# Kernel tuning notes

Hardware: AMD Instinct MI355X
Metric: run time of the kernel (lower is better)

## Reference

```python
import jax, jax.numpy as jnp
import numpy as np

BETA = 0.25
EPS = 1e-12

def normalise(x):
    # L2 normalise over last axis
    return x / jnp.sqrt(jnp.sum(x * x, axis=-1, keepdims=True) + EPS)

def setup_inputs() -> dict:
    key = jax.random.key(0)
    k = jax.random.split(key, 6)
    N, d, c, P = 8192, 768, 256, 16384
    return {
        "z": jax.random.normal(k[0], (N, d), dtype=jnp.float32),
        "W_in": jax.random.normal(k[1], (d, c), dtype=jnp.float32) * 0.02,
        "b_in": jnp.zeros((c,), dtype=jnp.float32),
        "W_out": jax.random.normal(k[2], (c, d), dtype=jnp.float32) * 0.02,
        "b_out": jnp.zeros((d,), dtype=jnp.float32),
        "codebook": jax.random.normal(k[3], (P, c), dtype=jnp.float32),
    }

def reference(z, W_in, b_in, W_out, b_out, codebook):
    sg = jax.lax.stop_gradient
    # input projection + L2 normalise
    zq = normalise(z @ W_in + b_in)                 # [N, c]
    cb = normalise(codebook)                        # [P, c]
    # squared euclidean distances: ||z||^2 - 2 z.c + ||c||^2
    dist = (jnp.sum(zq * zq, axis=-1, keepdims=True)
            - 2.0 * jnp.einsum('nc,pc->np', zq, cb)
            + jnp.sum(cb * cb, axis=-1)[None, :])   # [N, P]
    idxes = jnp.argmin(dist, axis=-1)               # [N]
    codes = normalise(codebook[idxes])              # gather + normalise, [N, c]
    loss = BETA * (zq - sg(codes)) ** 2 + (sg(zq) - codes) ** 2
    # straight-through estimator
    codes = zq + sg(codes - zq)
    out = codes @ W_out + b_out                     # [N, d]
    return out, loss, idxes
```

## Files before the change

### kernel.cpp

```cpp
#include <hip/hip_runtime.h>
#include <hip/hip_fp16.h>
#include <math.h>

#define NN 8192
#define DD 768
#define CC 256
#define PP 16384
#define NG 256
#define MARGIN 5.0e-3f
#define BETA_C 1.25f
#define EPS_C 1e-12f

typedef __attribute__((ext_vector_type(8))) _Float16 f16x8;
typedef __attribute__((ext_vector_type(8))) short bf16x8;
typedef __attribute__((ext_vector_type(4))) float f32x4;
typedef __attribute__((ext_vector_type(16))) float f32x16;

static __device__ __forceinline__ ushort f2h(float x) {
    _Float16 h = (_Float16)x;
    return __builtin_bit_cast(unsigned short, h);
}
static __device__ __forceinline__ ushort f2bf(float x) {
    unsigned u = __float_as_uint(x);
    return (ushort)((u + 0x7fffu + ((u >> 16) & 1u)) >> 16);
}

static __device__ __forceinline__ void gload_lds16(const void* g, void* l) {
    __builtin_amdgcn_global_load_lds(
        (const __attribute__((address_space(1))) unsigned int*)g,
        (__attribute__((address_space(3))) unsigned int*)l, 16, 0, 0);
}

__global__ __launch_bounds__(256) void k_gemm_in(const float* __restrict__ z,
    const float* __restrict__ W, const float* __restrict__ b,
    float* __restrict__ zq)
{
    __shared__ float zt[64][36];
    __shared__ float wt[32][68];
    const int t = threadIdx.x;
    const int ti = t >> 4, tj = t & 15;
    const int n0 = blockIdx.x * 64;
    const int c0 = blockIdx.y * 64;

    f32x4 acc[4];
#pragma unroll
    for (int r = 0; r < 4; ++r) acc[r] = (f32x4){0.f, 0.f, 0.f, 0.f};

    for (int k0 = 0; k0 < DD; k0 += 32) {
        __syncthreads();
#pragma unroll
        for (int l = 0; l < 2; ++l) {
            int idx = l * 256 + t;
            int row = idx >> 3, c4 = idx & 7;
            *reinterpret_cast<float4*>(&zt[row][c4 * 4]) =
                *reinterpret_cast<const float4*>(&z[(size_t)(n0 + row) * DD + k0 + c4 * 4]);
            int krow = idx >> 4, w4 = idx & 15;
            *reinterpret_cast<float4*>(&wt[krow][w4 * 4]) =
                *reinterpret_cast<const float4*>(&W[(size_t)(k0 + krow) * CC + c0 + w4 * 4]);
        }
        __syncthreads();
#pragma unroll
        for (int kk = 0; kk < 32; kk += 4) {
            float4 a4[4], b4[4];
#pragma unroll
            for (int r = 0; r < 4; ++r)
                a4[r] = *reinterpret_cast<const float4*>(&zt[ti * 4 + r][kk]);
#pragma unroll
            for (int q = 0; q < 4; ++q)
                b4[q] = *reinterpret_cast<const float4*>(&wt[kk + q][tj * 4]);
#pragma unroll
            for (int q = 0; q < 4; ++q)
#pragma unroll
                for (int r = 0; r < 4; ++r) {
                    float av = ((const float*)&a4[r])[q];
                    acc[r].x += av * b4[q].x;
                    acc[r].y += av * b4[q].y;
                    acc[r].z += av * b4[q].z;
                    acc[r].w += av * b4[q].w;
                }
        }
    }
#pragma unroll
    for (int r = 0; r < 4; ++r) {
        int col = c0 + tj * 4;
        float4 o;
        o.x = acc[r].x + b[col];
        o.y = acc[r].y + b[col + 1];
        o.z = acc[r].z + b[col + 2];
        o.w = acc[r].w + b[col + 3];
        *reinterpret_cast<float4*>(&zq[(size_t)(n0 + ti * 4 + r) * CC + col]) = o;
    }
}

__global__ __launch_bounds__(256) void k_norm2(const float* __restrict__ src,
    float* __restrict__ dstf32, ushort* __restrict__ dsth, int rows)
{
    const int wave = threadIdx.x >> 6;
    const int lane = threadIdx.x & 63;
    const int row = blockIdx.x * 4 + wave;
    if (row >= rows) return;
    float4 v = *reinterpret_cast<const float4*>(&src[(size_t)row * CC + lane * 4]);
    float s = v.x * v.x + v.y * v.y + v.z * v.z + v.w * v.w;
#pragma unroll
    for (int off = 32; off; off >>= 1) s += __shfl_xor(s, off, 64);
    float r = 1.0f / sqrtf(s + EPS_C);
    v.x *= r; v.y *= r; v.z *= r; v.w *= r;
    *reinterpret_cast<float4*>(&dstf32[(size_t)row * CC + lane * 4]) = v;
    ushort4 hv;
    hv.x = f2h(v.x); hv.y = f2h(v.y); hv.z = f2h(v.z); hv.w = f2h(v.w);
    *reinterpret_cast<ushort4*>(&dsth[(size_t)row * CC + lane * 4]) = hv;
}

__global__ __launch_bounds__(256) void k_prep(const float* __restrict__ codebook,
    ushort* __restrict__ cbh, float* __restrict__ cz2, float* __restrict__ rinv,
    const float* __restrict__ W, ushort* __restrict__ wthi)
{
    __shared__ float tile[64][68];
    const int t = threadIdx.x;
    if (blockIdx.x < 4096) {
        const int wave = t >> 6;
        const int lane = t & 63;
        const int row = blockIdx.x * 4 + wave;
        float4 v = *reinterpret_cast<const float4*>(&codebook[(size_t)row * CC + lane * 4]);
        float s = v.x * v.x + v.y * v.y + v.z * v.z + v.w * v.w;
#pragma unroll
        for (int off = 32; off; off >>= 1) s += __shfl_xor(s, off, 64);
        float r = 1.0f / sqrtf(s + EPS_C);
        v.x *= r; v.y *= r; v.z *= r; v.w *= r;
        ushort4 hv;
        hv.x = f2h(v.x); hv.y = f2h(v.y); hv.z = f2h(v.z); hv.w = f2h(v.w);
        *reinterpret_cast<ushort4*>(&cbh[(size_t)row * CC + lane * 4]) = hv;
        float s2 = v.x * v.x + v.y * v.y + v.z * v.z + v.w * v.w;
#pragma unroll
        for (int off = 32; off; off >>= 1) s2 += __shfl_xor(s2, off, 64);
        if (lane == 0) {
            cz2[row] = s2;
            rinv[row] = r;
        }
    } else {
        const int id = blockIdx.x - 4096;
        const int d0 = (id % 12) * 64;
        const int k0 = (id / 12) * 64;
#pragma unroll
        for (int i = 0; i < 16; ++i) {
            int row = i * 4 + (t >> 6);
            int col = t & 63;
            tile[row][col] = W[(size_t)(k0 + row) * DD + d0 + col];
        }
        __syncthreads();
#pragma unroll
        for (int i = 0; i < 16; ++i) {
            int drow = i * 4 + (t >> 6);
            int kc = t & 63;
            wthi[(size_t)(d0 + drow) * CC + k0 + kc] = f2bf(tile[kc][drow]);
        }
    }
}

__global__ __launch_bounds__(256, 4) void k_dist(
    const ushort* __restrict__ cbh, const ushort* __restrict__ zqh,
    const float* __restrict__ cz2,
    float* __restrict__ gmin, unsigned long long* __restrict__ maskA)
{
    __shared__ ushort lds[2][8192];
    const int t = threadIdx.x;
    const int lane = t & 63;
    const int w = t >> 6;
    const int wr = w >> 1;
    const int wc = w & 1;

    const int id = blockIdx.x;
    const int l = (id & 7) * 1024 + (id >> 3);
    const int p0 = (l >> 6) * 128;
    const int n0 = (l & 63) * 128;

    const int kh = lane >> 5;
    const int r31 = lane & 31;

    f32x16 acc[2][2];
#pragma unroll
    for (int mi = 0; mi < 2; ++mi) {
        const int pbm = p0 + wr * 64 + mi * 32;
#pragma unroll
        for (int q = 0; q < 4; ++q) {
            float4 cz = *reinterpret_cast<const float4*>(&cz2[pbm + q * 8 + kh * 4]);
#pragma unroll
            for (int j = 0; j < 4; ++j) {
                float v = -0.5f * ((const float*)&cz.x)[j];
                acc[mi][0][q * 4 + j] = v;
                acc[mi][1][q * 4 + j] = v;
            }
        }
    }

    const int u_l = lane >> 3;
    const int e = (lane & 7) ^ u_l;
    const int hh = e >> 2, jj = e & 3;
    const ushort* srcA[2];
    const ushort* srcB[2];
#pragma unroll
    for (int i = 0; i < 2; ++i)
        srcA[i] = cbh + (size_t)(p0 + 2 * (w * 16 + i * 8 + u_l) + hh) * CC + jj * 8;
#pragma unroll
    for (int i = 0; i < 2; ++i)
        srcB[i] = zqh + (size_t)(n0 + 2 * (w * 16 + i * 8 + u_l) + hh) * CC + jj * 8;

#define STAGE(BUF, KT)                                                        \
    {                                                                         \
        _Pragma("unroll")                                                     \
        for (int i = 0; i < 2; ++i)                                           \
            gload_lds16(srcA[i] + (KT) * 32, &lds[BUF][(w * 16 + i * 8) * 64]); \
        _Pragma("unroll")                                                     \
        for (int i = 0; i < 2; ++i)                                           \
            gload_lds16(srcB[i] + (KT) * 32, &lds[BUF][4096 + (w * 16 + i * 8) * 64]); \
    }

    const int ua = wr * 32 + (r31 >> 1);
    const int ub = wc * 32 + (r31 >> 1);
    const int hb = (r31 & 1) * 4 + kh;

#define COMPUTE(BUF)                                                          \
    {                                                                         \
        _Pragma("unroll")                                                     \
        for (int ks = 0; ks < 2; ++ks) {                                      \
            f16x8 af[2], bfv[2];                                              \
            _Pragma("unroll")                                                 \
            for (int mi = 0; mi < 2; ++mi) {                                  \
                int u = ua + mi * 16;                                         \
                af[mi] = *reinterpret_cast<const f16x8*>(                     \
                    &lds[BUF][u * 64 + (((hb + ks * 2) ^ (u & 7)) * 8)]);     \
            }                                                                 \
            _Pragma("unroll")                                                 \
            for (int ni = 0; ni < 2; ++ni) {                                  \
                int u = ub + ni * 16;                                         \
                bfv[ni] = *reinterpret_cast<const f16x8*>(                    \
                    &lds[BUF][4096 + u * 64 + (((hb + ks * 2) ^ (u & 7)) * 8)]); \
            }                                                                 \
            __builtin_amdgcn_s_setprio(1);                                    \
            acc[0][0] = __builtin_amdgcn_mfma_f32_32x32x16_f16(af[0], bfv[0], acc[0][0], 0, 0, 0); \
            acc[0][1] = __builtin_amdgcn_mfma_f32_32x32x16_f16(af[0], bfv[1], acc[0][1], 0, 0, 0); \
            acc[1][0] = __builtin_amdgcn_mfma_f32_32x32x16_f16(af[1], bfv[0], acc[1][0], 0, 0, 0); \
            acc[1][1] = __builtin_amdgcn_mfma_f32_32x32x16_f16(af[1], bfv[1], acc[1][1], 0, 0, 0); \
            __builtin_amdgcn_s_setprio(0);                                    \
        }                                                                     \
    }

#define BODY(KT, VM, DOSTAGE)                                                 \
    {                                                                         \
        if (DOSTAGE) STAGE(((KT) + 1) & 1, (KT) + 1);                         \
        __builtin_amdgcn_sched_barrier(0);                                    \
        asm volatile("s_waitcnt vmcnt(" #VM ")" ::: "memory");                \
        __builtin_amdgcn_s_barrier();                                         \
        __builtin_amdgcn_sched_barrier(0);                                    \
        COMPUTE((KT) & 1);                                                    \
        if ((KT) < 7) __builtin_amdgcn_s_barrier();                           \
    }

    STAGE(0, 0);
    BODY(0, 4, 1)
    BODY(1, 4, 1)
    BODY(2, 4, 1)
    BODY(3, 4, 1)
    BODY(4, 4, 1)
    BODY(5, 4, 1)
    BODY(6, 4, 1)
    BODY(7, 0, 0)

#undef BODY
#undef COMPUTE
#undef STAGE

#pragma unroll
    for (int ni = 0; ni < 2; ++ni) {
        float M = -1e30f;
#pragma unroll
        for (int mi = 0; mi < 2; ++mi)
#pragma unroll
            for (int r = 0; r < 16; ++r) M = fmaxf(M, acc[mi][ni][r]);
        M = fmaxf(M, __shfl_xor(M, 32, 64));
        const float thr = M - 0.5f * MARGIN;
        unsigned long long msk = 0ull;
#pragma unroll
        for (int mi = 0; mi < 2; ++mi)
#pragma unroll
            for (int q = 0; q < 4; ++q) {
                unsigned nib = 0u;
#pragma unroll
                for (int j = 0; j < 4; ++j)
                    nib |= (acc[mi][ni][q * 4 + j] >= thr) ? (1u << j) : 0u;
                msk |= (unsigned long long)nib << (mi * 32 + q * 8 + kh * 4);
            }
        msk |= __shfl_xor(msk, 32, 64);
        if (kh == 0) {
            int n = n0 + wc * 64 + ni * 32 + r31;
            int grp = (p0 >> 6) + wr;
            gmin[(size_t)n * NG + grp] = -2.0f * M;
            maskA[(size_t)n * NG + grp] = msk;
        }
    }
}

__global__ __launch_bounds__(256) void k_pick(
    const float* __restrict__ gmin, const unsigned long long* __restrict__ maskA,
    const float* __restrict__ zqn, const float* __restrict__ cb_raw,
    const float* __restrict__ rinv, const float* __restrict__ cz2,
    float* __restrict__ idxf, ushort* __restrict__ chi, float* __restrict__ loss)
{
    __shared__ int lst[4][256];
    __shared__ int cnt[4];
    const int t = threadIdx.x;
    const int w = t >> 6;
    const int lane = t & 63;
    const int row = blockIdx.x * 4 + w;

    float4 zr = *reinterpret_cast<const float4*>(&zqn[(size_t)row * CC + lane * 4]);
    float4 gv = *reinterpret_cast<const float4*>(&gmin[(size_t)row * NG + lane * 4]);

    float pm = fminf(fminf(gv.x, gv.y), fminf(gv.z, gv.w));
#pragma unroll
    for (int off = 1; off < 64; off <<= 1) pm = fminf(pm, __shfl_xor(pm, off, 64));
    const float thresh = pm + MARGIN;

    if (lane == 0) cnt[w] = 0;
    __syncthreads();
    {
        const float g4[4] = {gv.x, gv.y, gv.z, gv.w};
#pragma unroll
        for (int j = 0; j < 4; ++j)
            if (g4[j] <= thresh) {
                int pos = atomicAdd(&cnt[w], 1);
                lst[w][pos] = lane * 4 + j;
            }
    }
    __syncthreads();

    const int nc = cnt[w];
    unsigned long long best = ~0ull;
    for (int ci = 0; ci < nc; ++ci) {
        int g = lst[w][ci];
        unsigned long long msk = maskA[(size_t)row * NG + g];
        while (msk) {
            int bit = __ffsll((long long)msk) - 1;
            msk &= msk - 1;
            int p = g * 64 + bit;
            float rv = rinv[p];
            float4 c4 = *reinterpret_cast<const float4*>(&cb_raw[(size_t)p * CC + lane * 4]);
            float part = (c4.x * rv) * zr.x + (c4.y * rv) * zr.y
                       + (c4.z * rv) * zr.z + (c4.w * rv) * zr.w;
#pragma unroll
            for (int off = 1; off < 64; off <<= 1) part += __shfl_xor(part, off, 64);
            float d4 = fmaf(-2.0f, part, 4.0f + cz2[p]);
            unsigned long long pk = ((unsigned long long)__float_as_uint(d4) << 32) | (unsigned)p;
            best = best < pk ? best : pk;
        }
    }
    const int p = (int)(best & 0xffffffffu);
    if (lane == 0) idxf[row] = (float)p;

    const float rv = rinv[p];
    float4 cv = *reinterpret_cast<const float4*>(&cb_raw[(size_t)p * CC + lane * 4]);
    cv.x *= rv; cv.y *= rv; cv.z *= rv; cv.w *= rv;
    ushort4 hv;
    hv.x = f2bf(cv.x); hv.y = f2bf(cv.y); hv.z = f2bf(cv.z); hv.w = f2bf(cv.w);
    *reinterpret_cast<ushort4*>(&chi[(size_t)row * CC + lane * 4]) = hv;
    float4 lsv;
    float dx = zr.x - cv.x, dy = zr.y - cv.y, dz = zr.z - cv.z, dw = zr.w - cv.w;
    lsv.x = BETA_C * dx * dx; lsv.y = BETA_C * dy * dy;
    lsv.z = BETA_C * dz * dz; lsv.w = BETA_C * dw * dw;
    *reinterpret_cast<float4*>(&loss[(size_t)row * CC + lane * 4]) = lsv;
}

__global__ __launch_bounds__(256) void k_gemm_out_mfma(
    const ushort* __restrict__ chi, const ushort* __restrict__ wthi,
    const float* __restrict__ bout, float* __restrict__ out)
{
    __shared__ ushort sAh[128 * 64];
    __shared__ ushort sBh[128 * 64];
    const int t = threadIdx.x;
    const int lane = t & 63;
    const int w = t >> 6;
    const int wr = w >> 1;
    const int wc = w & 1;
    const int nb = blockIdx.x * 128;
    const int db = blockIdx.y * 128;
    const int kh = lane >> 5;
    const int r31 = lane & 31;

    f32x16 acc[2][2];
#pragma unroll
    for (int mi = 0; mi < 2; ++mi)
#pragma unroll
        for (int ni = 0; ni < 2; ++ni)
#pragma unroll
            for (int r = 0; r < 16; ++r) acc[mi][ni][r] = 0.f;

    const int srow = lane >> 3;
    const int schunk = (lane & 7) ^ srow;
    const size_t rowA = (size_t)(nb + w * 32 + srow) * CC;
    const size_t rowB = (size_t)(db + w * 32 + srow) * CC;
    const char* sAhsrc = (const char*)chi + rowA * 2 + schunk * 16;
    const char* sBhsrc = (const char*)wthi + rowB * 2 + schunk * 16;
    char* dA = (char*)sAh + (w * 32) * 128;
    char* dB = (char*)sBh + (w * 32) * 128;

    const int sx = (r31 & 7) << 4;

    for (int k0 = 0; k0 < CC; k0 += 64) {
        __syncthreads();
#pragma unroll
        for (int i = 0; i < 4; ++i) {
            gload_lds16(sAhsrc + (size_t)i * 8 * (CC * 2) + k0 * 2, dA + i * 1024);
            gload_lds16(sBhsrc + (size_t)i * 8 * (CC * 2) + k0 * 2, dB + i * 1024);
        }
        __syncthreads();
#pragma unroll
        for (int ks = 0; ks < 4; ++ks) {
            const int ko = ((ks * 32 + kh * 16) ^ sx);
            bf16x8 ah[2], bh[2];
#pragma unroll
            for (int mi = 0; mi < 2; ++mi)
                ah[mi] = *reinterpret_cast<const bf16x8*>(
                    (const char*)sAh + (wr * 64 + mi * 32 + r31) * 128 + ko);
#pragma unroll
            for (int ni = 0; ni < 2; ++ni)
                bh[ni] = *reinterpret_cast<const bf16x8*>(
                    (const char*)sBh + (wc * 64 + ni * 32 + r31) * 128 + ko);
#pragma unroll
            for (int mi = 0; mi < 2; ++mi)
#pragma unroll
                for (int ni = 0; ni < 2; ++ni)
                    acc[mi][ni] = __builtin_amdgcn_mfma_f32_32x32x16_bf16(
                        ah[mi], bh[ni], acc[mi][ni], 0, 0, 0);
        }
    }

#pragma unroll
    for (int ni = 0; ni < 2; ++ni) {
        const int d = db + wc * 64 + ni * 32 + r31;
        const float bv = bout[d];
#pragma unroll
        for (int mi = 0; mi < 2; ++mi) {
            const int nbase = nb + wr * 64 + mi * 32 + 4 * kh;
#pragma unroll
            for (int q = 0; q < 4; ++q)
#pragma unroll
                for (int j = 0; j < 4; ++j) {
                    int n = nbase + j + 8 * q;
                    out[(size_t)n * DD + d] = acc[mi][ni][q * 4 + j] + bv;
                }
        }
    }
}

extern "C" void kernel_launch(void* const* d_in, const int* in_sizes, int n_in,
                              void* d_out, int out_size, void* d_ws, size_t ws_size,
                              hipStream_t stream)
{
    const float* z        = (const float*)d_in[0];
    const float* W_in     = (const float*)d_in[1];
    const float* b_in     = (const float*)d_in[2];
    const float* W_out    = (const float*)d_in[3];
    const float* b_out    = (const float*)d_in[4];
    const float* codebook = (const float*)d_in[5];

    char* ws = (char*)d_ws;
    ushort* zqh   = (ushort*)(ws);
    ushort* cbh   = (ushort*)(ws + 4194304);
    ushort* chi   = (ushort*)(ws + 12582912);
    ushort* wthi  = (ushort*)(ws + 16777216);
    float*  cz2   = (float*)(ws + 17170432);
    float*  rinv  = (float*)(ws + 17235968);

    float* out  = (float*)d_out;
    float* loss = out + (size_t)NN * DD;
    float* idxf = loss + (size_t)NN * CC;

    float* gmin = (float*)d_out;
    unsigned long long* maskA = (unsigned long long*)((char*)d_out + 8388608);
    float* zq = loss;

    k_gemm_in<<<dim3(NN / 64, CC / 64), 256, 0, stream>>>(z, W_in, b_in, zq);
    k_norm2<<<NN / 4, 256, 0, stream>>>(zq, zq, zqh, NN);
    k_prep<<<PP / 4 + 48, 256, 0, stream>>>(codebook, cbh, cz2, rinv, W_out, wthi);
    k_dist<<<(PP / 128) * (NN / 128), 256, 0, stream>>>(cbh, zqh, cz2, gmin, maskA);
    k_pick<<<NN / 4, 256, 0, stream>>>(gmin, maskA, zq, codebook, rinv, cz2,
                                       idxf, chi, loss);
    k_gemm_out_mfma<<<dim3(NN / 128, DD / 128), 256, 0, stream>>>(chi, wthi, b_out, out);
}
```

Measured before the change: 192.3 us.

## Fuse input GEMM with L2 normalise and enlarge distance kernel P-tile

The input projection kernel now computes a full 256-wide row per block of 16 rows, so it can apply the bias, L2-normalise and write both fp32 and fp16 outputs directly. This removes the separate normalisation kernel and its extra round trip through global memory. The distance kernel's codebook tile is doubled from 128 to 256 rows, so each wave issues 8 MFMAs per k-step and zq tiles are reused more. In exchange it uses more registers and LDS, drops the occupancy hint and the block swizzle for L2 locality, and the input GEMM now does less work per thread and reloads the whole W slice in every block.

```diff
diff --git a/kernel.cpp b/kernel.cpp
--- a/kernel.cpp
+++ b/kernel.cpp
@@ -13,7 +13,6 @@
 
 typedef __attribute__((ext_vector_type(8))) _Float16 f16x8;
 typedef __attribute__((ext_vector_type(8))) short bf16x8;
-typedef __attribute__((ext_vector_type(4))) float f32x4;
 typedef __attribute__((ext_vector_type(16))) float f32x16;
 
 static __device__ __forceinline__ ushort f2h(float x) {
@@ -31,84 +30,84 @@
         (__attribute__((address_space(3))) unsigned int*)l, 16, 0, 0);
 }
 
-__global__ __launch_bounds__(256) void k_gemm_in(const float* __restrict__ z,
+__global__ __launch_bounds__(256) void k_gemm_in_norm(const float* __restrict__ z,
     const float* __restrict__ W, const float* __restrict__ b,
-    float* __restrict__ zq)
-{
-    __shared__ float zt[64][36];
-    __shared__ float wt[32][68];
+    float* __restrict__ zq, ushort* __restrict__ zqh)
+{
+    __shared__ float zt[16][36];
+    __shared__ float wt[32][260];
     const int t = threadIdx.x;
     const int ti = t >> 4, tj = t & 15;
-    const int n0 = blockIdx.x * 64;
-    const int c0 = blockIdx.y * 64;
-
-    f32x4 acc[4];
-#pragma unroll
-    for (int r = 0; r < 4; ++r) acc[r] = (f32x4){0.f, 0.f, 0.f, 0.f};
+    const int n0 = blockIdx.x * 16;
+
+    float acc[16];
+#pragma unroll
+    for (int c = 0; c < 16; ++c) acc[c] = 0.f;
 
     for (int k0 = 0; k0 < DD; k0 += 32) {
         __syncthreads();
-#pragma unroll
-        for (int l = 0; l < 2; ++l) {
-            int idx = l * 256 + t;
-            int row = idx >> 3, c4 = idx & 7;
+        if (t < 128) {
+            int row = t >> 3, c4 = t & 7;
             *reinterpret_cast<float4*>(&zt[row][c4 * 4]) =
                 *reinterpret_cast<const float4*>(&z[(size_t)(n0 + row) * DD + k0 + c4 * 4]);
-            int krow = idx >> 4, w4 = idx & 15;
+        }
+#pragma unroll
+        for (int l = 0; l < 8; ++l) {
+            int idx = l * 256 + t;
+            int krow = idx >> 6, w4 = idx & 63;
             *reinterpret_cast<float4*>(&wt[krow][w4 * 4]) =
-                *reinterpret_cast<const float4*>(&W[(size_t)(k0 + krow) * CC + c0 + w4 * 4]);
+                *reinterpret_cast<const float4*>(&W[(size_t)(k0 + krow) * CC + w4 * 4]);
         }
         __syncthreads();
 #pragma unroll
         for (int kk = 0; kk < 32; kk += 4) {
-            float4 a4[4], b4[4];
-#pragma unroll
-            for (int r = 0; r < 4; ++r)
-                a4[r] = *reinterpret_cast<const float4*>(&zt[ti * 4 + r][kk]);
-#pragma unroll
-            for (int q = 0; q < 4; ++q)
-                b4[q] = *reinterpret_cast<const float4*>(&wt[kk + q][tj * 4]);
-#pragma unroll
-            for (int q = 0; q < 4; ++q)
-#pragma unroll
-                for (int r = 0; r < 4; ++r) {
-                    float av = ((const float*)&a4[r])[q];
-                    acc[r].x += av * b4[q].x;
-                    acc[r].y += av * b4[q].y;
-                    acc[r].z += av * b4[q].z;
-                    acc[r].w += av * b4[q].w;
+            float4 a4 = *reinterpret_cast<const float4*>(&zt[ti][kk]);
+#pragma unroll
+            for (int q = 0; q < 4; ++q) {
+                float av = ((const float*)&a4)[q];
+#pragma unroll
+                for (int c = 0; c < 4; ++c) {
+                    float4 wv = *reinterpret_cast<const float4*>(&wt[kk + q][c * 64 + tj * 4]);
+                    acc[c * 4 + 0] += av * wv.x;
+                    acc[c * 4 + 1] += av * wv.y;
+                    acc[c * 4 + 2] += av * wv.z;
+                    acc[c * 4 + 3] += av * wv.w;
                 }
-        }
-    }
-#pragma unroll
-    for (int r = 0; r < 4; ++r) {
-        int col = c0 + tj * 4;
-        float4 o;
-        o.x = acc[r].x + b[col];
-        o.y = acc[r].y + b[col + 1];
-        o.z = acc[r].z + b[col + 2];
-        o.w = acc[r].w + b[col + 3];
-        *reinterpret_cast<float4*>(&zq[(size_t)(n0 + ti * 4 + r) * CC + col]) = o;
-    }
-}
-
-__global__ __launch_bounds__(256) void k_norm2(const float* __restrict__ src,
-    float* __restrict__ dstf32, ushort* __restrict__ dsth, int rows)
-{
-    const int wave = threadIdx.x >> 6;
-    const int lane = threadIdx.x & 63;
-    const int row = blockIdx.x * 4 + wave;
-    if (row >= rows) return;
-    float4 v = *reinterpret_cast<const float4*>(&src[(size_t)row * CC + lane * 4]);
-    float s = v.x * v.x + v.y * v.y + v.z * v.z + v.w * v.w;
-#pragma unroll
-    for (int off = 32; off; off >>= 1) s += __shfl_xor(s, off, 64);
-    float r = 1.0f / sqrtf(s + EPS_C);
-    v.x *= r; v.y *= r; v.z *= r; v.w *= r;
-    *reinterpret_cast<float4*>(&dstf32[(size_t)row * CC + lane * 4]) = v;
-    ushort4 hv;
-    hv.x = f2h(v.x); hv.y = f2h(v.y); hv.z = f2h(v.z); hv.w = f2h(v.w);
-    *reinterpret_cast<ushort4*>(&dsth[(size_t)row * CC + lane * 4]) = hv;
+            }
+        }
+    }
+
+    float p[4];
+#pragma unroll
+    for (int c = 0; c < 4; ++c) {
+        const int col = c * 64 + tj * 4;
+        acc[c * 4 + 0] += b[col + 0];
+        acc[c * 4 + 1] += b[col + 1];
+        acc[c * 4 + 2] += b[col + 2];
+        acc[c * 4 + 3] += b[col + 3];
+        p[c] = acc[c * 4 + 0] * acc[c * 4 + 0] + acc[c * 4 + 1] * acc[c * 4 + 1]
+             + acc[c * 4 + 2] * acc[c * 4 + 2] + acc[c * 4 + 3] * acc[c * 4 + 3];
+    }
+    float s0 = p[0] + p[2];
+    float s1 = p[1] + p[3];
+    float s = s0 + s1;
+#pragma unroll
+    for (int off = 8; off; off >>= 1) s += __shfl_xor(s, off, 64);
+    const float r = 1.0f / sqrtf(s + EPS_C);
+
+#pragma unroll
+    for (int c = 0; c < 4; ++c) {
+        const int col = c * 64 + tj * 4;
+        float4 v;
+        v.x = acc[c * 4 + 0] * r;
+        v.y = acc[c * 4 + 1] * r;
+        v.z = acc[c * 4 + 2] * r;
+        v.w = acc[c * 4 + 3] * r;
+        *reinterpret_cast<float4*>(&zq[(size_t)(n0 + ti) * CC + col]) = v;
+        ushort4 hv;
+        hv.x = f2h(v.x); hv.y = f2h(v.y); hv.z = f2h(v.z); hv.w = f2h(v.w);
+        *reinterpret_cast<ushort4*>(&zqh[(size_t)(n0 + ti) * CC + col]) = hv;
+    }
 }
 
 __global__ __launch_bounds__(256) void k_prep(const float* __restrict__ codebook,
@@ -157,30 +156,26 @@
     }
 }
 
-__global__ __launch_bounds__(256, 4) void k_dist(
+__global__ __launch_bounds__(256) void k_dist(
     const ushort* __restrict__ cbh, const ushort* __restrict__ zqh,
     const float* __restrict__ cz2,
     float* __restrict__ gmin, unsigned long long* __restrict__ maskA)
 {
-    __shared__ ushort lds[2][8192];
+    __shared__ ushort lds[2][12288];
     const int t = threadIdx.x;
     const int lane = t & 63;
     const int w = t >> 6;
     const int wr = w >> 1;
     const int wc = w & 1;
-
-    const int id = blockIdx.x;
-    const int l = (id & 7) * 1024 + (id >> 3);
-    const int p0 = (l >> 6) * 128;
-    const int n0 = (l & 63) * 128;
-
+    const int p0 = blockIdx.x * 256;
+    const int n0 = blockIdx.y * 128;
     const int kh = lane >> 5;
     const int r31 = lane & 31;
 
-    f32x16 acc[2][2];
-#pragma unroll
-    for (int mi = 0; mi < 2; ++mi) {
-        const int pbm = p0 + wr * 64 + mi * 32;
+    f32x16 acc[4][2];
+#pragma unroll
+    for (int mi = 0; mi < 4; ++mi) {
+        const int pbm = p0 + wr * 128 + mi * 32;
 #pragma unroll
         for (int q = 0; q < 4; ++q) {
             float4 cz = *reinterpret_cast<const float4*>(&cz2[pbm + q * 8 + kh * 4]);
@@ -196,11 +191,11 @@
     const int u_l = lane >> 3;
     const int e = (lane & 7) ^ u_l;
     const int hh = e >> 2, jj = e & 3;
-    const ushort* srcA[2];
+    const ushort* srcA[4];
     const ushort* srcB[2];
 #pragma unroll
-    for (int i = 0; i < 2; ++i)
-        srcA[i] = cbh + (size_t)(p0 + 2 * (w * 16 + i * 8 + u_l) + hh) * CC + jj * 8;
+    for (int i = 0; i < 4; ++i)
+        srcA[i] = cbh + (size_t)(p0 + 2 * (w * 32 + i * 8 + u_l) + hh) * CC + jj * 8;
 #pragma unroll
     for (int i = 0; i < 2; ++i)
         srcB[i] = zqh + (size_t)(n0 + 2 * (w * 16 + i * 8 + u_l) + hh) * CC + jj * 8;
@@ -208,14 +203,14 @@
 #define STAGE(BUF, KT)                                                        \
     {                                                                         \
         _Pragma("unroll")                                                     \
-        for (int i = 0; i < 2; ++i)                                           \
-            gload_lds16(srcA[i] + (KT) * 32, &lds[BUF][(w * 16 + i * 8) * 64]); \
+        for (int i = 0; i < 4; ++i)                                           \
+            gload_lds16(srcA[i] + (KT) * 32, &lds[BUF][(w * 32 + i * 8) * 64]); \
         _Pragma("unroll")                                                     \
         for (int i = 0; i < 2; ++i)                                           \
-            gload_lds16(srcB[i] + (KT) * 32, &lds[BUF][4096 + (w * 16 + i * 8) * 64]); \
-    }
-
-    const int ua = wr * 32 + (r31 >> 1);
+            gload_lds16(srcB[i] + (KT) * 32, &lds[BUF][8192 + (w * 16 + i * 8) * 64]); \
+    }
+
+    const int ua = wr * 64 + (r31 >> 1);
     const int ub = wc * 32 + (r31 >> 1);
     const int hb = (r31 & 1) * 4 + kh;
 
@@ -223,9 +218,9 @@
     {                                                                         \
         _Pragma("unroll")                                                     \
         for (int ks = 0; ks < 2; ++ks) {                                      \
-            f16x8 af[2], bfv[2];                                              \
+            f16x8 af[4], bfv[2];                                              \
             _Pragma("unroll")                                                 \
-            for (int mi = 0; mi < 2; ++mi) {                                  \
+            for (int mi = 0; mi < 4; ++mi) {                                  \
                 int u = ua + mi * 16;                                         \
                 af[mi] = *reinterpret_cast<const f16x8*>(                     \
                     &lds[BUF][u * 64 + (((hb + ks * 2) ^ (u & 7)) * 8)]);     \
@@ -234,13 +229,17 @@
             for (int ni = 0; ni < 2; ++ni) {                                  \
                 int u = ub + ni * 16;                                         \
                 bfv[ni] = *reinterpret_cast<const f16x8*>(                    \
-                    &lds[BUF][4096 + u * 64 + (((hb + ks * 2) ^ (u & 7)) * 8)]); \
+                    &lds[BUF][8192 + u * 64 + (((hb + ks * 2) ^ (u & 7)) * 8)]); \
             }                                                                 \
             __builtin_amdgcn_s_setprio(1);                                    \
             acc[0][0] = __builtin_amdgcn_mfma_f32_32x32x16_f16(af[0], bfv[0], acc[0][0], 0, 0, 0); \
             acc[0][1] = __builtin_amdgcn_mfma_f32_32x32x16_f16(af[0], bfv[1], acc[0][1], 0, 0, 0); \
             acc[1][0] = __builtin_amdgcn_mfma_f32_32x32x16_f16(af[1], bfv[0], acc[1][0], 0, 0, 0); \
             acc[1][1] = __builtin_amdgcn_mfma_f32_32x32x16_f16(af[1], bfv[1], acc[1][1], 0, 0, 0); \
+            acc[2][0] = __builtin_amdgcn_mfma_f32_32x32x16_f16(af[2], bfv[0], acc[2][0], 0, 0, 0); \
+            acc[2][1] = __builtin_amdgcn_mfma_f32_32x32x16_f16(af[2], bfv[1], acc[2][1], 0, 0, 0); \
+            acc[3][0] = __builtin_amdgcn_mfma_f32_32x32x16_f16(af[3], bfv[0], acc[3][0], 0, 0, 0); \
+            acc[3][1] = __builtin_amdgcn_mfma_f32_32x32x16_f16(af[3], bfv[1], acc[3][1], 0, 0, 0); \
             __builtin_amdgcn_s_setprio(0);                                    \
         }                                                                     \
     }
@@ -257,13 +256,13 @@
     }
 
     STAGE(0, 0);
-    BODY(0, 4, 1)
-    BODY(1, 4, 1)
-    BODY(2, 4, 1)
-    BODY(3, 4, 1)
-    BODY(4, 4, 1)
-    BODY(5, 4, 1)
-    BODY(6, 4, 1)
+    BODY(0, 6, 1)
+    BODY(1, 6, 1)
+    BODY(2, 6, 1)
+    BODY(3, 6, 1)
+    BODY(4, 6, 1)
+    BODY(5, 6, 1)
+    BODY(6, 6, 1)
     BODY(7, 0, 0)
 
 #undef BODY
@@ -272,30 +271,33 @@
 
 #pragma unroll
     for (int ni = 0; ni < 2; ++ni) {
-        float M = -1e30f;
-#pragma unroll
-        for (int mi = 0; mi < 2; ++mi)
-#pragma unroll
-            for (int r = 0; r < 16; ++r) M = fmaxf(M, acc[mi][ni][r]);
-        M = fmaxf(M, __shfl_xor(M, 32, 64));
-        const float thr = M - 0.5f * MARGIN;
-        unsigned long long msk = 0ull;
-#pragma unroll
-        for (int mi = 0; mi < 2; ++mi)
-#pragma unroll
-            for (int q = 0; q < 4; ++q) {
-                unsigned nib = 0u;
-#pragma unroll
-                for (int j = 0; j < 4; ++j)
-                    nib |= (acc[mi][ni][q * 4 + j] >= thr) ? (1u << j) : 0u;
-                msk |= (unsigned long long)nib << (mi * 32 + q * 8 + kh * 4);
+#pragma unroll
+        for (int g = 0; g < 2; ++g) {
+            float M = -1e30f;
+#pragma unroll
+            for (int m2 = 0; m2 < 2; ++m2)
+#pragma unroll
+                for (int r = 0; r < 16; ++r) M = fmaxf(M, acc[g * 2 + m2][ni][r]);
+            M = fmaxf(M, __shfl_xor(M, 32, 64));
+            const float thr = M - 0.5f * MARGIN;
+            unsigned long long msk = 0ull;
+#pragma unroll
+            for (int m2 = 0; m2 < 2; ++m2)
+#pragma unroll
+                for (int q = 0; q < 4; ++q) {
+                    unsigned nib = 0u;
+#pragma unroll
+                    for (int j = 0; j < 4; ++j)
+                        nib |= (acc[g * 2 + m2][ni][q * 4 + j] >= thr) ? (1u << j) : 0u;
+                    msk |= (unsigned long long)nib << (m2 * 32 + q * 8 + kh * 4);
+                }
+            msk |= __shfl_xor(msk, 32, 64);
+            if (kh == 0) {
+                int n = n0 + wc * 64 + ni * 32 + r31;
+                int grp = (p0 >> 6) + wr * 2 + g;
+                gmin[(size_t)n * NG + grp] = -2.0f * M;
+                maskA[(size_t)n * NG + grp] = msk;
             }
-        msk |= __shfl_xor(msk, 32, 64);
-        if (kh == 0) {
-            int n = n0 + wc * 64 + ni * 32 + r31;
-            int grp = (p0 >> 6) + wr;
-            gmin[(size_t)n * NG + grp] = -2.0f * M;
-            maskA[(size_t)n * NG + grp] = msk;
         }
     }
 }
@@ -479,10 +481,9 @@
     unsigned long long* maskA = (unsigned long long*)((char*)d_out + 8388608);
     float* zq = loss;
 
-    k_gemm_in<<<dim3(NN / 64, CC / 64), 256, 0, stream>>>(z, W_in, b_in, zq);
-    k_norm2<<<NN / 4, 256, 0, stream>>>(zq, zq, zqh, NN);
+    k_gemm_in_norm<<<NN / 16, 256, 0, stream>>>(z, W_in, b_in, zq, zqh);
     k_prep<<<PP / 4 + 48, 256, 0, stream>>>(codebook, cbh, cz2, rinv, W_out, wthi);
-    k_dist<<<(PP / 128) * (NN / 128), 256, 0, stream>>>(cbh, zqh, cz2, gmin, maskA);
+    k_dist<<<dim3(PP / 256, NN / 128), 256, 0, stream>>>(cbh, zqh, cz2, gmin, maskA);
     k_pick<<<NN / 4, 256, 0, stream>>>(gmin, maskA, zq, codebook, rinv, cz2,
                                        idxf, chi, loss);
     k_gemm_out_mfma<<<dim3(NN / 128, DD / 128), 256, 0, stream>>>(chi, wthi, b_out, out);
```

New measurement: 229.2 us. 19.2% more time.
